# Performance work log

Hardware: AMD Instinct MI355X
Metric: run time of the kernel (lower is better)

Reference implementation:

```python
import jax, jax.numpy as jnp
import numpy as np

N_NODES = 50000
N_EDGES = 800000
IN_CH = 128
HID = 256
N_GRAPHS = 512


def setup_inputs() -> dict:
    key = jax.random.key(0)
    ks = jax.random.split(key, 10)
    x = jax.random.normal(ks[0], (N_NODES, IN_CH), dtype=jnp.float32)
    edge_index = jax.random.randint(ks[1], (2, N_EDGES), 0, N_NODES, dtype=jnp.int32)
    batch = jnp.sort(jax.random.randint(ks[2], (N_NODES,), 0, N_GRAPHS, dtype=jnp.int32))
    # GCNConv params (glorot-ish init)
    W0 = jax.random.normal(ks[3], (IN_CH, HID), dtype=jnp.float32) / np.sqrt(IN_CH)
    b0 = jnp.zeros((HID,), dtype=jnp.float32)
    W1 = jax.random.normal(ks[4], (HID, HID), dtype=jnp.float32) / np.sqrt(HID)
    b1 = jnp.zeros((HID,), dtype=jnp.float32)
    W2 = jax.random.normal(ks[5], (HID, HID), dtype=jnp.float32) / np.sqrt(HID)
    b2 = jnp.zeros((HID,), dtype=jnp.float32)
    return {"x": x, "W0": W0, "b0": b0, "W1": W1, "b1": b1, "W2": W2, "b2": b2,
            "edge_index": edge_index, "batch": batch}


def _gcn_norm(edge_index, num_nodes):
    # PyG gcn_norm with add_self_loops=True: A_hat = A + I, norm = D^-1/2 A_hat D^-1/2
    src, dst = edge_index[0], edge_index[1]
    loop = jnp.arange(num_nodes, dtype=src.dtype)
    src = jnp.concatenate([src, loop])
    dst = jnp.concatenate([dst, loop])
    deg = jax.ops.segment_sum(jnp.ones_like(dst, dtype=jnp.float32), dst,
                              num_segments=num_nodes)
    dinv = jnp.where(deg > 0, jax.lax.rsqrt(deg), 0.0)
    norm = dinv[src] * dinv[dst]  # [E + N]
    return src, dst, norm


def _gcn_conv(x, W, b, src, dst, norm, num_nodes):
    h = x @ W                                  # [N, out]
    msg = norm[:, None] * h[src]               # gather + scale, [E+N, out]
    out = jax.ops.segment_sum(msg, dst, num_segments=num_nodes)  # scatter-add
    return out + b


def reference(x, W0, b0, W1, b1, W2, b2, edge_index, batch):
    n = x.shape[0]
    src, dst, norm = _gcn_norm(edge_index, n)  # normalization is layer-independent
    h = jax.nn.relu(_gcn_conv(x, W0, b0, src, dst, norm, n))
    h = jax.nn.relu(_gcn_conv(h, W1, b1, src, dst, norm, n))
    h = jax.nn.relu(_gcn_conv(h, W2, b2, src, dst, norm, n))
    # global_add_pool: segment-sum node features by graph id
    return jax.ops.segment_sum(h, batch, num_segments=N_GRAPHS)
```

## Files before the change

kernel.cpp:

```cpp
#include <hip/hip_runtime.h>
#include <hip/hip_fp16.h>

constexpr int NN  = 50000;
constexpr int NE  = 800000;
constexpr int CIN = 128;
constexpr int CH  = 256;
constexpr int NG  = 512;

typedef unsigned short ushort_t;
typedef unsigned int uint_t;
typedef unsigned char uchar_t;
typedef __attribute__((ext_vector_type(2))) float f32x2_t;
typedef __attribute__((ext_vector_type(2))) uint_t u32x2_t;

static __device__ __forceinline__ ushort_t f2bf(float f) {
    uint_t u = __float_as_uint(f);
    u += 0x7fffu + ((u >> 16) & 1u);
    return (ushort_t)(u >> 16);
}

static __device__ __forceinline__ float h16tof(uint_t bits) {
    return __half2float(__ushort_as_half((unsigned short)bits));
}

__global__ void conv_x_kernel(const float4* __restrict__ x, ushort4* __restrict__ xb, int n4) {
    int i = blockIdx.x * blockDim.x + threadIdx.x;
    if (i >= n4) return;
    float4 v = x[i];
    ushort4 o;
    o.x = f2bf(v.x); o.y = f2bf(v.y); o.z = f2bf(v.z); o.w = f2bf(v.w);
    xb[i] = o;
}

__global__ void conv_wt3_kernel(const float* __restrict__ W0, const float* __restrict__ W1,
                                const float* __restrict__ W2, ushort_t* __restrict__ W0t,
                                ushort_t* __restrict__ W1t, ushort_t* __restrict__ W2t) {
    int i = blockIdx.x * blockDim.x + threadIdx.x;
    if (i < 32768) {
        int k = i >> 8, n = i & 255;
        W0t[n * 128 + k] = f2bf(W0[i]);
    } else if (i < 98304) {
        int j = i - 32768;
        int k = j >> 8, n = j & 255;
        W1t[n * 256 + k] = f2bf(W1[j]);
    } else if (i < 163840) {
        int j = i - 98304;
        int k = j >> 8, n = j & 255;
        W2t[n * 256 + k] = f2bf(W2[j]);
    }
}

__global__ void count_kernel(const int* __restrict__ dst, int* __restrict__ cnt, int E) {
    int e = blockIdx.x * blockDim.x + threadIdx.x;
    if (e < E) atomicAdd(&cnt[dst[e]], 1);
}

__global__ __launch_bounds__(256) void scan_bsum_kernel(const int* __restrict__ cnt,
                                                        int* __restrict__ bsum, int n) {
    int i = blockIdx.x * 256 + threadIdx.x;
    int v = (i < n) ? ((cnt[i] + 7) & ~7) : 0;
    #pragma unroll
    for (int off = 32; off >= 1; off >>= 1) v += __shfl_xor(v, off, 64);
    __shared__ int ws[4];
    if ((threadIdx.x & 63) == 0) ws[threadIdx.x >> 6] = v;
    __syncthreads();
    if (threadIdx.x == 0) bsum[blockIdx.x] = ws[0] + ws[1] + ws[2] + ws[3];
}

__global__ __launch_bounds__(256) void scan_boff_kernel(int* __restrict__ bsum, int nb) {
    int tid = threadIdx.x, lane = tid & 63, wid = tid >> 6;
    int v = (tid < nb) ? bsum[tid] : 0;
    int s = v;
    #pragma unroll
    for (int off = 1; off < 64; off <<= 1) {
        int t = __shfl_up(s, off, 64);
        if (lane >= off) s += t;
    }
    __shared__ int wsum[4];
    if (lane == 63) wsum[wid] = s;
    __syncthreads();
    int wadd = 0;
    #pragma unroll
    for (int w = 0; w < 4; w++) if (w < wid) wadd += wsum[w];
    if (tid < nb) bsum[tid] = wadd + s - v;
}

__global__ __launch_bounds__(256) void scan_final_kernel(const int* __restrict__ cnt,
                                                         const int* __restrict__ boff,
                                                         int* __restrict__ rowptr,
                                                         float* __restrict__ dinv, int n) {
    int tid = threadIdx.x, lane = tid & 63, wid = tid >> 6;
    int i = blockIdx.x * 256 + tid;
    int c = (i < n) ? cnt[i] : 0;
    int v = (c + 7) & ~7;
    int s = v;
    #pragma unroll
    for (int off = 1; off < 64; off <<= 1) {
        int t = __shfl_up(s, off, 64);
        if (lane >= off) s += t;
    }
    __shared__ int wsum[4];
    if (lane == 63) wsum[wid] = s;
    __syncthreads();
    int wadd = boff[blockIdx.x];
    #pragma unroll
    for (int w = 0; w < 4; w++) if (w < wid) wadd += wsum[w];
    if (i < n) {
        rowptr[i] = wadd + s - v;
        dinv[i]   = rsqrtf((float)c + 1.0f);
        if (i == n - 1) rowptr[n] = wadd + s;
    }
}

__global__ void scatter_kernel(const int* __restrict__ src, const int* __restrict__ dst,
                               const int* __restrict__ rowptr, int* __restrict__ cursor,
                               const float* __restrict__ dinv, uint_t* __restrict__ epack, int E) {
    int e = blockIdx.x * blockDim.x + threadIdx.x;
    if (e >= E) return;
    int d = dst[e];
    int s = src[e];
    int p = rowptr[d] + atomicAdd(&cursor[d], 1);
    uint_t hb = (uint_t)__half_as_ushort(__float2half(dinv[s]));
    epack[p] = (uint_t)s | (hb << 16);
}

template <int C, int MODE>
__global__ __launch_bounds__(256) void node_agg_kernel(
    const ushort_t* __restrict__ h, const int* __restrict__ rowptr,
    const int* __restrict__ degc, const uint_t* __restrict__ epack,
    const float* __restrict__ dinv, const float* __restrict__ bias,
    const int* __restrict__ batch, void* __restrict__ out_v, int n) {
    constexpr int V = C / 64;
    int wave = threadIdx.x >> 6;
    int lane = threadIdx.x & 63;
    int d = blockIdx.x * 4 + wave;
    if (d >= n) return;

    int beg = __builtin_amdgcn_readfirstlane(rowptr[d]);
    int deg = __builtin_amdgcn_readfirstlane(degc[d]);
    const uint_t* hu = (const uint_t*)h;

    float acc[V] = {};
    const uint4* ep4 = (const uint4*)(epack + beg);
    uint4 ea, eb, na, nb;
    if (deg > 0) { ea = ep4[0]; eb = ep4[1]; }

    for (int e = 0; e < deg; e += 8) {
        int blk = e >> 3;
        if (e + 8 < deg) { na = ep4[blk * 2 + 2]; nb = ep4[blk * 2 + 3]; }
        uint_t eps[8] = {ea.x, ea.y, ea.z, ea.w, eb.x, eb.y, eb.z, eb.w};
        int   srcs[8];
        float wts[8];
        #pragma unroll
        for (int u = 0; u < 8; u++) {
            bool a = (e + u) < deg;
            srcs[u] = a ? (int)(eps[u] & 0xffffu) : d;
            wts[u]  = a ? h16tof(eps[u] >> 16) : 0.0f;
        }
        if constexpr (V == 4) {
            uint_t ra[8], rb[8];
            #pragma unroll
            for (int u = 0; u < 8; u++) {
                const uint_t* row = hu + (size_t)__builtin_amdgcn_readfirstlane(srcs[u]) * (C / 2);
                ra[u] = row[lane];
                rb[u] = row[64 + lane];
            }
            #pragma unroll
            for (int u = 0; u < 8; u++) {
                float w = wts[u];
                acc[0] += w * __uint_as_float(ra[u] << 16);
                acc[1] += w * __uint_as_float(ra[u] & 0xffff0000u);
                acc[2] += w * __uint_as_float(rb[u] << 16);
                acc[3] += w * __uint_as_float(rb[u] & 0xffff0000u);
            }
        } else {
            uint_t rv[8];
            #pragma unroll
            for (int u = 0; u < 8; u++) {
                const uint_t* row = hu + (size_t)__builtin_amdgcn_readfirstlane(srcs[u]) * (C / 2);
                rv[u] = row[lane];
            }
            #pragma unroll
            for (int u = 0; u < 8; u++) {
                float w = wts[u];
                acc[0] += w * __uint_as_float(rv[u] << 16);
                acc[1] += w * __uint_as_float(rv[u] & 0xffff0000u);
            }
        }
        ea = na; eb = nb;
    }

    float dd = dinv[d];
    float self[V];
    {
        const uint_t* row = hu + (size_t)d * (C / 2);
        uint_t sa = row[lane];
        self[0] = __uint_as_float(sa << 16);
        self[1] = __uint_as_float(sa & 0xffff0000u);
        if constexpr (V == 4) {
            uint_t sb = row[64 + lane];
            self[2] = __uint_as_float(sb << 16);
            self[3] = __uint_as_float(sb & 0xffff0000u);
        }
    }

    float r[V];
    if constexpr (MODE >= 1) {
        float2 bA = *(const float2*)(bias + 2 * lane);
        r[0] = fmaxf(dd * acc[0] + dd * dd * self[0] + bA.x, 0.0f);
        r[1] = fmaxf(dd * acc[1] + dd * dd * self[1] + bA.y, 0.0f);
        if constexpr (V == 4) {
            float2 bB = *(const float2*)(bias + 128 + 2 * lane);
            r[2] = fmaxf(dd * acc[2] + dd * dd * self[2] + bB.x, 0.0f);
            r[3] = fmaxf(dd * acc[3] + dd * dd * self[3] + bB.y, 0.0f);
        }
    } else {
        #pragma unroll
        for (int i = 0; i < V; i++)
            r[i] = dd * acc[i] + dd * dd * self[i];
    }

    if constexpr (MODE == 2) {
        float* o = (float*)out_v + (size_t)batch[d] * C;
        atomicAdd(o + 2 * lane, r[0]);
        atomicAdd(o + 2 * lane + 1, r[1]);
        if constexpr (V == 4) {
            atomicAdd(o + 128 + 2 * lane, r[2]);
            atomicAdd(o + 128 + 2 * lane + 1, r[3]);
        }
    } else {
        uint_t* o = (uint_t*)((ushort_t*)out_v + (size_t)d * C);
        __builtin_nontemporal_store((uint_t)f2bf(r[0]) | ((uint_t)f2bf(r[1]) << 16), &o[lane]);
        if constexpr (V == 4)
            __builtin_nontemporal_store((uint_t)f2bf(r[2]) | ((uint_t)f2bf(r[3]) << 16), &o[64 + lane]);
    }
}

template <int MODE>
__global__ __launch_bounds__(256) void node_agg_fp8_kernel(
    const uchar_t* __restrict__ h8, const int* __restrict__ rowptr,
    const int* __restrict__ degc, const uint_t* __restrict__ epack,
    const float* __restrict__ dinv, const float* __restrict__ bias,
    const int* __restrict__ batch, void* __restrict__ out_v, int n) {
    int wave = threadIdx.x >> 6;
    int lane = threadIdx.x & 63;
    int d = blockIdx.x * 4 + wave;
    if (d >= n) return;

    int beg = __builtin_amdgcn_readfirstlane(rowptr[d]);
    int deg = __builtin_amdgcn_readfirstlane(degc[d]);
    const uint_t* hu = (const uint_t*)h8;
    const uint4* ep4 = (const uint4*)(epack + beg);

    float a0 = 0.0f, a1 = 0.0f, a2 = 0.0f, a3 = 0.0f;
    int nblk = (deg + 7) >> 3;

    uint4 ec0, ec1;
    uint4 en0, en1;
    uint_t rvC[8];
    uint_t rvN[8];

    if (nblk > 0) {
        ec0 = ep4[0]; ec1 = ep4[1];
        uint_t eps[8] = {ec0.x, ec0.y, ec0.z, ec0.w, ec1.x, ec1.y, ec1.z, ec1.w};
        #pragma unroll
        for (int u = 0; u < 8; u++) {
            int s = (u < deg) ? (int)(eps[u] & 0xffffu) : d;
            rvC[u] = hu[(size_t)__builtin_amdgcn_readfirstlane(s) * 64 + lane];
        }
        if (nblk > 1) { en0 = ep4[2]; en1 = ep4[3]; }
    }

    for (int b = 0; b < nblk; b++) {
        int e = b * 8;
        uint4 ef0, ef1;
        if (b + 2 < nblk) { ef0 = ep4[(b + 2) * 2]; ef1 = ep4[(b + 2) * 2 + 1]; }
        if (b + 1 < nblk) {
            uint_t eps[8] = {en0.x, en0.y, en0.z, en0.w, en1.x, en1.y, en1.z, en1.w};
            #pragma unroll
            for (int u = 0; u < 8; u++) {
                int s = (e + 8 + u < deg) ? (int)(eps[u] & 0xffffu) : d;
                rvN[u] = hu[(size_t)__builtin_amdgcn_readfirstlane(s) * 64 + lane];
            }
        }
        {
            uint_t eps[8] = {ec0.x, ec0.y, ec0.z, ec0.w, ec1.x, ec1.y, ec1.z, ec1.w};
            #pragma unroll
            for (int u = 0; u < 8; u++) {
                float w = (e + u < deg) ? h16tof(eps[u] >> 16) : 0.0f;
                f32x2_t lo = __builtin_amdgcn_cvt_pk_f32_fp8(rvC[u], false);
                f32x2_t hi = __builtin_amdgcn_cvt_pk_f32_fp8(rvC[u], true);
                a0 += w * lo.x;
                a1 += w * lo.y;
                a2 += w * hi.x;
                a3 += w * hi.y;
            }
        }
        ec0 = en0; ec1 = en1; en0 = ef0; en1 = ef1;
        #pragma unroll
        for (int u = 0; u < 8; u++) rvC[u] = rvN[u];
    }

    float dd = dinv[d];
    float dd2 = dd * dd;
    uint_t sv = hu[(size_t)d * 64 + lane];
    f32x2_t slo = __builtin_amdgcn_cvt_pk_f32_fp8(sv, false);
    f32x2_t shi = __builtin_amdgcn_cvt_pk_f32_fp8(sv, true);

    float4 b4 = *(const float4*)(bias + 4 * lane);
    float r0 = fmaxf(dd * a0 + dd2 * slo.x + b4.x, 0.0f);
    float r1 = fmaxf(dd * a1 + dd2 * slo.y + b4.y, 0.0f);
    float r2 = fmaxf(dd * a2 + dd2 * shi.x + b4.z, 0.0f);
    float r3 = fmaxf(dd * a3 + dd2 * shi.y + b4.w, 0.0f);

    if constexpr (MODE == 2) {
        float* o = (float*)out_v + (size_t)batch[d] * CH + 4 * lane;
        atomicAdd(o + 0, r0);
        atomicAdd(o + 1, r1);
        atomicAdd(o + 2, r2);
        atomicAdd(o + 3, r3);
    } else {
        u32x2_t st;
        st.x = (uint_t)f2bf(r0) | ((uint_t)f2bf(r1) << 16);
        st.y = (uint_t)f2bf(r2) | ((uint_t)f2bf(r3) << 16);
        *((u32x2_t*)((ushort_t*)out_v + (size_t)d * CH) + lane) = st;
    }
}

typedef __attribute__((ext_vector_type(8))) short bf16x8;
typedef __attribute__((ext_vector_type(4))) float f32x4;

template <int MODE, int F8OUT>
__global__ __launch_bounds__(256) void gemm_bf16_kernel(
    const ushort_t* __restrict__ A, const ushort_t* __restrict__ Wt,
    const float* __restrict__ bias, void* __restrict__ Cv, int M, int K) {
    __shared__ union alignas(16) {
        ushort_t ab[2][128][40];
        uchar_t  f8[128][128];
    } smem;
    int tid = threadIdx.x;
    int row0 = blockIdx.x * 128, col0 = blockIdx.y * 128;
    int lr = tid >> 2, lq = tid & 3;
    int lane = tid & 63, wv = tid >> 6;
    int wr = (wv >> 1) * 64, wc = (wv & 1) * 64;
    int r16 = lane & 15, quad = lane >> 4;

    f32x4 acc[4][4] = {};

    for (int k0 = 0; k0 < K; k0 += 32) {
        {
            int gr0 = row0 + lr, gr1 = row0 + lr + 64;
            uint4 a0 = make_uint4(0, 0, 0, 0), a1 = make_uint4(0, 0, 0, 0);
            if (gr0 < M) a0 = *(const uint4*)(A + (size_t)gr0 * K + k0 + lq * 8);
            if (gr1 < M) a1 = *(const uint4*)(A + (size_t)gr1 * K + k0 + lq * 8);
            *(uint4*)&smem.ab[0][lr][lq * 8]      = a0;
            *(uint4*)&smem.ab[0][lr + 64][lq * 8] = a1;
            uint4 b0 = *(const uint4*)(Wt + (size_t)(col0 + lr) * K + k0 + lq * 8);
            uint4 b1 = *(const uint4*)(Wt + (size_t)(col0 + lr + 64) * K + k0 + lq * 8);
            *(uint4*)&smem.ab[1][lr][lq * 8]      = b0;
            *(uint4*)&smem.ab[1][lr + 64][lq * 8] = b1;
        }
        __syncthreads();
        bf16x8 af[4], bfr[4];
        #pragma unroll
        for (int i = 0; i < 4; i++) af[i]  = *(const bf16x8*)&smem.ab[0][wr + i * 16 + r16][quad * 8];
        #pragma unroll
        for (int j = 0; j < 4; j++) bfr[j] = *(const bf16x8*)&smem.ab[1][wc + j * 16 + r16][quad * 8];
        #pragma unroll
        for (int i = 0; i < 4; i++)
            #pragma unroll
            for (int j = 0; j < 4; j++)
                acc[i][j] = __builtin_amdgcn_mfma_f32_16x16x32_bf16(af[i], bfr[j], acc[i][j], 0, 0, 0);
        __syncthreads();
    }

    if constexpr (F8OUT) {
        #pragma unroll
        for (int j = 0; j < 4; j++) {
            int colt = wc + j * 16 + r16;
            #pragma unroll
            for (int i = 0; i < 4; i++) {
                #pragma unroll
                for (int r = 0; r < 4; r++) {
                    float v = acc[i][j][r];
                    uint_t pk = __builtin_amdgcn_cvt_pk_fp8_f32(v, v, 0u, false);
                    smem.f8[wr + i * 16 + quad * 4 + r][colt] = (uchar_t)(pk & 0xffu);
                }
            }
        }
        __syncthreads();
        uchar_t* C8 = (uchar_t*)Cv;
        #pragma unroll
        for (int k = 0; k < 4; k++) {
            int idx = k * 256 + tid;
            int r = idx >> 3, coff = (idx & 7) * 16;
            if (row0 + r < M)
                *(uint4*)(C8 + (size_t)(row0 + r) * 256 + col0 + coff) =
                    *(const uint4*)&smem.f8[r][coff];
        }
    } else {
        #pragma unroll
        for (int j = 0; j < 4; j++) {
            int colc = col0 + wc + j * 16 + r16;
            float bval = (MODE == 1) ? bias[colc] : 0.0f;
            #pragma unroll
            for (int i = 0; i < 4; i++) {
                #pragma unroll
                for (int r = 0; r < 4; r++) {
                    int row = row0 + wr + i * 16 + quad * 4 + r;
                    if (row < M) {
                        float v = acc[i][j][r];
                        if (MODE == 1) v = fmaxf(v + bval, 0.0f);
                        ((ushort_t*)Cv)[(size_t)row * 256 + colc] = f2bf(v);
                    }
                }
            }
        }
    }
}

extern "C" void kernel_launch(void* const* d_in, const int* in_sizes, int n_in,
                              void* d_out, int out_size, void* d_ws, size_t ws_size,
                              hipStream_t stream) {
    const float* x   = (const float*)d_in[0];
    const float* W0  = (const float*)d_in[1];
    const float* b0  = (const float*)d_in[2];
    const float* W1  = (const float*)d_in[3];
    const float* b1  = (const float*)d_in[4];
    const float* W2  = (const float*)d_in[5];
    const float* b2  = (const float*)d_in[6];
    const int*   ei  = (const int*)d_in[7];
    const int*   src = ei;
    const int*   dst = ei + NE;
    const int*   batch = (const int*)d_in[8];
    float* out = (float*)d_out;

    char* ws = (char*)d_ws;
    ushort_t* P1  = (ushort_t*)ws;
    ushort_t* G0  = (ushort_t*)(ws + 25600000ull);
    uchar_t*  F8  = (uchar_t*) (ws + 38400000ull);
    ushort_t* xbf = (ushort_t*)(ws + 51200000ull);
    ushort_t* W0t = (ushort_t*)(ws + 64000000ull);
    ushort_t* W1t = (ushort_t*)(ws + 64065536ull);
    ushort_t* W2t = (ushort_t*)(ws + 64196608ull);
    float*    dinv   = (float*)(ws + 64327680ull);
    int*      rowptr = (int*)  (ws + 64527680ull);
    int*      cnt    = (int*)  (ws + 64727808ull);
    uint_t*   epack  = (uint_t*)(ws + 64927808ull);
    int*      bsum   = (int*)  (ws + 71327808ull);
    int*      cursor = (int*)ws;

    const int scanBlocks = (NN + 255) / 256;
    const int nodeBlocks = (NN + 3) / 4;
    const dim3 ggrid((NN + 127) / 128, 2);

    conv_x_kernel<<<(NN * CIN / 4 + 255) / 256, 256, 0, stream>>>((const float4*)x, (ushort4*)xbf, NN * CIN / 4);
    conv_wt3_kernel<<<640, 256, 0, stream>>>(W0, W1, W2, W0t, W1t, W2t);

    hipMemsetAsync(cnt, 0, (size_t)NN * 4, stream);
    count_kernel<<<(NE + 255) / 256, 256, 0, stream>>>(dst, cnt, NE);
    scan_bsum_kernel<<<scanBlocks, 256, 0, stream>>>(cnt, bsum, NN);
    scan_boff_kernel<<<1, 256, 0, stream>>>(bsum, scanBlocks);
    scan_final_kernel<<<scanBlocks, 256, 0, stream>>>(cnt, bsum, rowptr, dinv, NN);
    hipMemsetAsync(cursor, 0, (size_t)NN * 4, stream);
    scatter_kernel<<<(NE + 255) / 256, 256, 0, stream>>>(src, dst, rowptr, cursor, dinv, epack, NE);

    node_agg_kernel<CIN, 0><<<nodeBlocks, 256, 0, stream>>>(xbf, rowptr, cnt, epack, dinv, nullptr, nullptr, G0, NN);
    gemm_bf16_kernel<1, 0><<<ggrid, 256, 0, stream>>>(G0, W0t, b0, P1, NN, CIN);

    gemm_bf16_kernel<0, 1><<<ggrid, 256, 0, stream>>>(P1, W1t, nullptr, F8, NN, CH);
    node_agg_fp8_kernel<1><<<nodeBlocks, 256, 0, stream>>>(F8, rowptr, cnt, epack, dinv, b1, nullptr, P1, NN);

    gemm_bf16_kernel<0, 1><<<ggrid, 256, 0, stream>>>(P1, W2t, nullptr, F8, NN, CH);
    hipMemsetAsync(out, 0, (size_t)NG * CH * 4, stream);
    node_agg_fp8_kernel<2><<<nodeBlocks, 256, 0, stream>>>(F8, rowptr, cnt, epack, dinv, b2, batch, out, NN);
}
```

Before: 491.7 us.

## Process two destination nodes per wave in FP8 aggregation kernel

The FP8 neighbor-aggregation kernel now gives each wavefront two destination nodes and interleaves their gathers, replacing the previous software-pipelined single-node loop with prefetch of the next edge block. The aim is more independent memory loads in flight per wave and half as many blocks. In exchange, the explicit cross-iteration prefetch is gone, the shorter-degree node wastes gathers on padding (it reloads its last block and its dummy gathers read node dA) until the longer one finishes, and register pressure rises.

```diff
diff --git a/kernel.cpp b/kernel.cpp
--- a/kernel.cpp
+++ b/kernel.cpp
@@ -244,86 +244,124 @@
     const int* __restrict__ batch, void* __restrict__ out_v, int n) {
     int wave = threadIdx.x >> 6;
     int lane = threadIdx.x & 63;
-    int d = blockIdx.x * 4 + wave;
-    if (d >= n) return;
-
-    int beg = __builtin_amdgcn_readfirstlane(rowptr[d]);
-    int deg = __builtin_amdgcn_readfirstlane(degc[d]);
+    int dA = (blockIdx.x * 4 + wave) * 2;
+    if (dA >= n) return;
+    int dB = dA + 1;
+    bool hasB = dB < n;
+    if (!hasB) dB = dA;
+
+    int begA = __builtin_amdgcn_readfirstlane(rowptr[dA]);
+    int degA = __builtin_amdgcn_readfirstlane(degc[dA]);
+    int begB = __builtin_amdgcn_readfirstlane(rowptr[dB]);
+    int degB = hasB ? __builtin_amdgcn_readfirstlane(degc[dB]) : 0;
+
     const uint_t* hu = (const uint_t*)h8;
-    const uint4* ep4 = (const uint4*)(epack + beg);
-
-    float a0 = 0.0f, a1 = 0.0f, a2 = 0.0f, a3 = 0.0f;
-    int nblk = (deg + 7) >> 3;
-
-    uint4 ec0, ec1;
-    uint4 en0, en1;
-    uint_t rvC[8];
-    uint_t rvN[8];
-
-    if (nblk > 0) {
-        ec0 = ep4[0]; ec1 = ep4[1];
-        uint_t eps[8] = {ec0.x, ec0.y, ec0.z, ec0.w, ec1.x, ec1.y, ec1.z, ec1.w};
+    const uint4* epq = (const uint4*)epack;
+
+    int nbA = (degA + 7) >> 3;
+    int nbB = (degB + 7) >> 3;
+    int nbMax = max(nbA, nbB);
+
+    float aA0 = 0.0f, aA1 = 0.0f, aA2 = 0.0f, aA3 = 0.0f;
+    float aB0 = 0.0f, aB1 = 0.0f, aB2 = 0.0f, aB3 = 0.0f;
+
+    for (int b = 0; b < nbMax; b++) {
+        int boA = min(b, max(nbA - 1, 0));
+        int boB = min(b, max(nbB - 1, 0));
+        uint4 eA0 = epq[(begA >> 2) + boA * 2];
+        uint4 eA1 = epq[(begA >> 2) + boA * 2 + 1];
+        uint4 eB0 = epq[(begB >> 2) + boB * 2];
+        uint4 eB1 = epq[(begB >> 2) + boB * 2 + 1];
+
+        uint_t epsA[8] = {eA0.x, eA0.y, eA0.z, eA0.w, eA1.x, eA1.y, eA1.z, eA1.w};
+        uint_t epsB[8] = {eB0.x, eB0.y, eB0.z, eB0.w, eB1.x, eB1.y, eB1.z, eB1.w};
+        float wA[8], wB[8];
+
+        uint_t rvA[8];
         #pragma unroll
         for (int u = 0; u < 8; u++) {
-            int s = (u < deg) ? (int)(eps[u] & 0xffffu) : d;
-            rvC[u] = hu[(size_t)__builtin_amdgcn_readfirstlane(s) * 64 + lane];
-        }
-        if (nblk > 1) { en0 = ep4[2]; en1 = ep4[3]; }
-    }
-
-    for (int b = 0; b < nblk; b++) {
-        int e = b * 8;
-        uint4 ef0, ef1;
-        if (b + 2 < nblk) { ef0 = ep4[(b + 2) * 2]; ef1 = ep4[(b + 2) * 2 + 1]; }
-        if (b + 1 < nblk) {
-            uint_t eps[8] = {en0.x, en0.y, en0.z, en0.w, en1.x, en1.y, en1.z, en1.w};
-            #pragma unroll
-            for (int u = 0; u < 8; u++) {
-                int s = (e + 8 + u < deg) ? (int)(eps[u] & 0xffffu) : d;
-                rvN[u] = hu[(size_t)__builtin_amdgcn_readfirstlane(s) * 64 + lane];
-            }
-        }
-        {
-            uint_t eps[8] = {ec0.x, ec0.y, ec0.z, ec0.w, ec1.x, ec1.y, ec1.z, ec1.w};
-            #pragma unroll
-            for (int u = 0; u < 8; u++) {
-                float w = (e + u < deg) ? h16tof(eps[u] >> 16) : 0.0f;
-                f32x2_t lo = __builtin_amdgcn_cvt_pk_f32_fp8(rvC[u], false);
-                f32x2_t hi = __builtin_amdgcn_cvt_pk_f32_fp8(rvC[u], true);
-                a0 += w * lo.x;
-                a1 += w * lo.y;
-                a2 += w * hi.x;
-                a3 += w * hi.y;
-            }
-        }
-        ec0 = en0; ec1 = en1; en0 = ef0; en1 = ef1;
-        #pragma unroll
-        for (int u = 0; u < 8; u++) rvC[u] = rvN[u];
-    }
-
-    float dd = dinv[d];
-    float dd2 = dd * dd;
-    uint_t sv = hu[(size_t)d * 64 + lane];
-    f32x2_t slo = __builtin_amdgcn_cvt_pk_f32_fp8(sv, false);
-    f32x2_t shi = __builtin_amdgcn_cvt_pk_f32_fp8(sv, true);
+            bool act = (b * 8 + u) < degA;
+            int s = act ? (int)(epsA[u] & 0xffffu) : dA;
+            wA[u] = act ? h16tof(epsA[u] >> 16) : 0.0f;
+            rvA[u] = hu[(size_t)__builtin_amdgcn_readfirstlane(s) * 64 + lane];
+        }
+        uint_t rvB[8];
+        #pragma unroll
+        for (int u = 0; u < 8; u++) {
+            bool act = (b * 8 + u) < degB;
+            int s = act ? (int)(epsB[u] & 0xffffu) : dA;
+            wB[u] = act ? h16tof(epsB[u] >> 16) : 0.0f;
+            rvB[u] = hu[(size_t)__builtin_amdgcn_readfirstlane(s) * 64 + lane];
+        }
+        #pragma unroll
+        for (int u = 0; u < 8; u++) {
+            float w = wA[u];
+            f32x2_t lo = __builtin_amdgcn_cvt_pk_f32_fp8(rvA[u], false);
+            f32x2_t hi = __builtin_amdgcn_cvt_pk_f32_fp8(rvA[u], true);
+            aA0 += w * lo.x;
+            aA1 += w * lo.y;
+            aA2 += w * hi.x;
+            aA3 += w * hi.y;
+        }
+        #pragma unroll
+        for (int u = 0; u < 8; u++) {
+            float w = wB[u];
+            f32x2_t lo = __builtin_amdgcn_cvt_pk_f32_fp8(rvB[u], false);
+            f32x2_t hi = __builtin_amdgcn_cvt_pk_f32_fp8(rvB[u], true);
+            aB0 += w * lo.x;
+            aB1 += w * lo.y;
+            aB2 += w * hi.x;
+            aB3 += w * hi.y;
+        }
+    }
 
     float4 b4 = *(const float4*)(bias + 4 * lane);
-    float r0 = fmaxf(dd * a0 + dd2 * slo.x + b4.x, 0.0f);
-    float r1 = fmaxf(dd * a1 + dd2 * slo.y + b4.y, 0.0f);
-    float r2 = fmaxf(dd * a2 + dd2 * shi.x + b4.z, 0.0f);
-    float r3 = fmaxf(dd * a3 + dd2 * shi.y + b4.w, 0.0f);
-
-    if constexpr (MODE == 2) {
-        float* o = (float*)out_v + (size_t)batch[d] * CH + 4 * lane;
-        atomicAdd(o + 0, r0);
-        atomicAdd(o + 1, r1);
-        atomicAdd(o + 2, r2);
-        atomicAdd(o + 3, r3);
-    } else {
-        u32x2_t st;
-        st.x = (uint_t)f2bf(r0) | ((uint_t)f2bf(r1) << 16);
-        st.y = (uint_t)f2bf(r2) | ((uint_t)f2bf(r3) << 16);
-        *((u32x2_t*)((ushort_t*)out_v + (size_t)d * CH) + lane) = st;
+
+    {
+        float dd = dinv[dA];
+        float dd2 = dd * dd;
+        uint_t sv = hu[(size_t)dA * 64 + lane];
+        f32x2_t slo = __builtin_amdgcn_cvt_pk_f32_fp8(sv, false);
+        f32x2_t shi = __builtin_amdgcn_cvt_pk_f32_fp8(sv, true);
+        float r0 = fmaxf(dd * aA0 + dd2 * slo.x + b4.x, 0.0f);
+        float r1 = fmaxf(dd * aA1 + dd2 * slo.y + b4.y, 0.0f);
+        float r2 = fmaxf(dd * aA2 + dd2 * shi.x + b4.z, 0.0f);
+        float r3 = fmaxf(dd * aA3 + dd2 * shi.y + b4.w, 0.0f);
+        if constexpr (MODE == 2) {
+            float* o = (float*)out_v + (size_t)batch[dA] * CH + 4 * lane;
+            atomicAdd(o + 0, r0);
+            atomicAdd(o + 1, r1);
+            atomicAdd(o + 2, r2);
+            atomicAdd(o + 3, r3);
+        } else {
+            u32x2_t st;
+            st.x = (uint_t)f2bf(r0) | ((uint_t)f2bf(r1) << 16);
+            st.y = (uint_t)f2bf(r2) | ((uint_t)f2bf(r3) << 16);
+            *((u32x2_t*)((ushort_t*)out_v + (size_t)dA * CH) + lane) = st;
+        }
+    }
+    if (hasB) {
+        float dd = dinv[dB];
+        float dd2 = dd * dd;
+        uint_t sv = hu[(size_t)dB * 64 + lane];
+        f32x2_t slo = __builtin_amdgcn_cvt_pk_f32_fp8(sv, false);
+        f32x2_t shi = __builtin_amdgcn_cvt_pk_f32_fp8(sv, true);
+        float r0 = fmaxf(dd * aB0 + dd2 * slo.x + b4.x, 0.0f);
+        float r1 = fmaxf(dd * aB1 + dd2 * slo.y + b4.y, 0.0f);
+        float r2 = fmaxf(dd * aB2 + dd2 * shi.x + b4.z, 0.0f);
+        float r3 = fmaxf(dd * aB3 + dd2 * shi.y + b4.w, 0.0f);
+        if constexpr (MODE == 2) {
+            float* o = (float*)out_v + (size_t)batch[dB] * CH + 4 * lane;
+            atomicAdd(o + 0, r0);
+            atomicAdd(o + 1, r1);
+            atomicAdd(o + 2, r2);
+            atomicAdd(o + 3, r3);
+        } else {
+            u32x2_t st;
+            st.x = (uint_t)f2bf(r0) | ((uint_t)f2bf(r1) << 16);
+            st.y = (uint_t)f2bf(r2) | ((uint_t)f2bf(r3) << 16);
+            *((u32x2_t*)((ushort_t*)out_v + (size_t)dB * CH) + lane) = st;
+        }
     }
 }
 
@@ -452,6 +490,7 @@
 
     const int scanBlocks = (NN + 255) / 256;
     const int nodeBlocks = (NN + 3) / 4;
+    const int nodeBlocks2 = (NN + 7) / 8;
     const dim3 ggrid((NN + 127) / 128, 2);
 
     conv_x_kernel<<<(NN * CIN / 4 + 255) / 256, 256, 0, stream>>>((const float4*)x, (ushort4*)xbf, NN * CIN / 4);
@@ -469,9 +508,9 @@
     gemm_bf16_kernel<1, 0><<<ggrid, 256, 0, stream>>>(G0, W0t, b0, P1, NN, CIN);
 
     gemm_bf16_kernel<0, 1><<<ggrid, 256, 0, stream>>>(P1, W1t, nullptr, F8, NN, CH);
-    node_agg_fp8_kernel<1><<<nodeBlocks, 256, 0, stream>>>(F8, rowptr, cnt, epack, dinv, b1, nullptr, P1, NN);
+    node_agg_fp8_kernel<1><<<nodeBlocks2, 256, 0, stream>>>(F8, rowptr, cnt, epack, dinv, b1, nullptr, P1, NN);
 
     gemm_bf16_kernel<0, 1><<<ggrid, 256, 0, stream>>>(P1, W2t, nullptr, F8, NN, CH);
     hipMemsetAsync(out, 0, (size_t)NG * CH * 4, stream);
-    node_agg_fp8_kernel<2><<<nodeBlocks, 256, 0, stream>>>(F8, rowptr, cnt, epack, dinv, b2, batch, out, NN);
-}
+    node_agg_fp8_kernel<2><<<nodeBlocks2, 256, 0, stream>>>(F8, rowptr, cnt, epack, dinv, b2, batch, out, NN);
+}
```

New measurement: 490.2 us. About the same (-0.3%).
